# Performance work log

Measured on AMD Instinct MI355X. Metric: run time of the kernel, lower is better.

## Reference

```python
import jax, jax.numpy as jnp
import numpy as np

B = 1; H = 192; W = 192; DIM = 128; HEADS = 8
WS = 16                      # window_size
OWS = 24                     # overlap_win_size = int(16*0.5)+16
PAD = 4                      # (OWS-WS)//2
C2 = DIM // 2                # per-branch channels
H2 = HEADS // 2              # per-branch heads
HID = 256                    # mlp_ratio * dim
TBL = (WS + OWS - 1) ** 2    # 1521 rel-pos table entries
SCALE = (C2 // H2) ** (-0.5) # head_dim ** -0.5


def layer_norm(x, w, b, eps=1e-5):
    mu = jnp.mean(x, -1, keepdims=True)
    var = jnp.mean((x - mu) ** 2, -1, keepdims=True)
    return (x - mu) * jax.lax.rsqrt(var + eps) * w + b


def window_partition(x, ws):
    b, h, w, c = x.shape
    x = x.reshape(b, h // ws, ws, w // ws, ws, c).transpose(0, 1, 3, 2, 4, 5)
    return x.reshape(-1, ws, ws, c)


def window_reverse(win, ws, h, w):
    b = win.shape[0] // ((h // ws) * (w // ws))
    x = win.reshape(b, h // ws, w // ws, ws, ws, -1).transpose(0, 1, 3, 2, 4, 5)
    return x.reshape(b, h, w, -1)


def _patch_idx(h, w):
    ri = (jnp.arange(h // WS) * WS)[:, None] + jnp.arange(OWS)  # (nwh, OWS)
    ci = (jnp.arange(w // WS) * WS)[:, None] + jnp.arange(OWS)  # (nww, OWS)
    return ri, ci


def unfold_patches(x):
    # x: (b, h, w, c) -> (b*nw, OWS*OWS, c); matches nn.Unfold(OWS, stride=WS, pad=PAD)
    b, h, w, c = x.shape
    xp = jnp.pad(x, ((0, 0), (PAD, PAD), (PAD, PAD), (0, 0)))
    ri, ci = _patch_idx(h, w)
    p = xp[:, ri[:, None, :, None], ci[None, :, None, :], :]  # (b,nwh,nww,OWS,OWS,c)
    return p.reshape(-1, OWS * OWS, c)


def fold_patches(p, b, h, w):
    # inverse of unfold: scatter-add overlapping patches into (b, h+2PAD, w+2PAD, c)
    nwh, nww = h // WS, w // WS
    c = p.shape[-1]
    p = p.reshape(b, nwh, nww, OWS, OWS, c)
    ri, ci = _patch_idx(h, w)
    canvas = jnp.zeros((b, h + 2 * PAD, w + 2 * PAD, c), p.dtype)
    return canvas.at[:, ri[:, None, :, None], ci[None, :, None, :], :].add(p)


def cubic_kernel(x, A=-0.75):
    # PyTorch bicubic (cubic convolution, A=-0.75)
    ax = jnp.abs(x)
    w1 = ((A + 2.0) * ax - (A + 3.0)) * ax * ax + 1.0
    w2 = A * (ax * (ax * (ax - 5.0) + 8.0) - 4.0)
    return jnp.where(ax <= 1.0, w1, jnp.where(ax < 2.0, w2, 0.0))


def resize_matrix(n_out, n_in):
    # dense 1-D bicubic resize matrix, align_corners=False, border-clamped (torch semantics)
    i = jnp.arange(n_out, dtype=jnp.float32)
    src = (i + 0.5) * (float(n_in) / float(n_out)) - 0.5
    fl = jnp.floor(src)
    idx = fl[:, None] + jnp.arange(-1, 3, dtype=jnp.float32)[None, :]  # (n_out, 4)
    wts = cubic_kernel(src[:, None] - idx)
    idx_c = jnp.clip(idx, 0, n_in - 1).astype(jnp.int32)
    M = jnp.zeros((n_out, n_in), jnp.float32)
    return M.at[jnp.arange(n_out)[:, None], idx_c].add(wts)


def cross_attn(xq, xkv, rpi, wq, wkv, rpb):
    b_, nq, d = xq.shape
    n = xkv.shape[1]
    q = (xq @ wq).reshape(b_, nq, H2, -1).transpose(0, 2, 1, 3)
    k, v = jnp.split(xkv @ wkv, 2, axis=-1)
    k = k.reshape(b_, n, H2, -1).transpose(0, 2, 1, 3)
    v = v.reshape(b_, n, H2, -1).transpose(0, 2, 1, 3)
    attn = jnp.einsum('bhqd,bhkd->bhqk', q * SCALE, k)
    bias = rpb[rpi.reshape(-1)].reshape(WS * WS, OWS * OWS, H2)
    bias = bias.transpose(2, 0, 1) if nq < n else bias.transpose(2, 1, 0)
    attn = jax.nn.softmax(attn + bias[None], axis=-1)
    out = jnp.einsum('bhqk,bhkd->bhqd', attn, v)
    return out.transpose(0, 2, 1, 3).reshape(b_, nq, d)


def gsfn(x, h, w, fc1_w, fc1_b, sgn_w, sgn_b, conv_w, conv_b, fc2_w, fc2_b):
    x = x @ fc1_w + fc1_b  # NOTE: source GSFN never applies self.act
    x1, x2 = jnp.split(x, 2, axis=-1)
    Bn, N, Ch = x2.shape
    x2 = layer_norm(x2, sgn_w, sgn_b).transpose(0, 2, 1).reshape(Bn, Ch, h, w)
    x2 = jax.lax.conv_general_dilated(
        x2, conv_w, (1, 1), ((1, 1), (1, 1)),
        feature_group_count=Ch, dimension_numbers=('NCHW', 'OIHW', 'NCHW'))
    x2 = x2 + conv_b[None, :, None, None]
    x2 = x2.reshape(Bn, Ch, N).transpose(0, 2, 1)
    return (x1 * x2) @ fc2_w + fc2_b


def mstb(x_tkn, ln1_w, ln1_b, q1_w, kv1_w, rpb1, q2_w, kv2_w, rpb2,
         proj_w, proj_b, ln2_w, ln2_b, fc1_w, fc1_b, sgn_w, sgn_b,
         conv_w, conv_b, fc2_w, fc2_b, rpi, h, w):
    b, _, c = x_tkn.shape
    short = x_tkn
    x = layer_norm(x_tkn, ln1_w, ln1_b).reshape(b, h, w, c)
    xw = window_partition(x, WS).reshape(-1, WS * WS, c)     # (b*nw, ws*ws, c)
    xa, xb = jnp.split(xw, 2, axis=-1)
    xb_img = window_reverse(xb.reshape(-1, WS, WS, C2), WS, h, w)  # (b,h,w,C2)
    xb_p = unfold_patches(xb_img)                            # (b*nw, OWS*OWS, C2)
    a = cross_attn(xa, xb_p, rpi, q1_w, kv1_w, rpb1) + xa
    bb = cross_attn(xb_p, xa, rpi, q2_w, kv2_w, rpb2) + xb_p
    folded = fold_patches(bb, b, h, w)                       # (b, h+2p, w+2p, C2)
    Mh = resize_matrix(h, h + 2 * PAD)
    Mw = resize_matrix(w, w + 2 * PAD)
    resized = jnp.einsum('oi,bijc,pj->bopc', Mh, folded, Mw)  # bicubic to (h,w)
    xb2 = window_partition(resized, WS).reshape(-1, WS * WS, C2)
    x = jnp.concatenate([a, xb2], -1)
    x = window_reverse(x.reshape(-1, WS, WS, c), WS, h, w).reshape(b, h * w, c)
    x = x @ proj_w + proj_b + short
    x = gsfn(layer_norm(x, ln2_w, ln2_b), h, w, fc1_w, fc1_b,
             sgn_w, sgn_b, conv_w, conv_b, fc2_w, fc2_b) + x
    return x


def setup_inputs() -> dict:
    key = jax.random.key(0)
    ks = jax.random.split(key, 12)
    rn = lambda k, s, sc: jax.random.normal(k, s, jnp.float32) * sc
    return {
        'x_tkn': jax.random.normal(ks[0], (B, H * W, DIM), jnp.float32),
        'ln1_w': jnp.ones((DIM,), jnp.float32), 'ln1_b': jnp.zeros((DIM,), jnp.float32),
        'q1_w': rn(ks[1], (C2, C2), 0.05), 'kv1_w': rn(ks[2], (C2, 2 * C2), 0.05),
        'rpb1': rn(ks[3], (TBL, H2), 0.02),
        'q2_w': rn(ks[4], (C2, C2), 0.05), 'kv2_w': rn(ks[5], (C2, 2 * C2), 0.05),
        'rpb2': rn(ks[6], (TBL, H2), 0.02),
        'proj_w': rn(ks[7], (DIM, DIM), 0.05), 'proj_b': jnp.zeros((DIM,), jnp.float32),
        'ln2_w': jnp.ones((DIM,), jnp.float32), 'ln2_b': jnp.zeros((DIM,), jnp.float32),
        'fc1_w': rn(ks[8], (DIM, HID), 0.05), 'fc1_b': jnp.zeros((HID,), jnp.float32),
        'sgn_w': jnp.ones((HID // 2,), jnp.float32), 'sgn_b': jnp.zeros((HID // 2,), jnp.float32),
        'conv_w': rn(ks[9], (HID // 2, 1, 3, 3), 0.1), 'conv_b': jnp.zeros((HID // 2,), jnp.float32),
        'fc2_w': rn(ks[10], (HID // 2, DIM), 0.05), 'fc2_b': jnp.zeros((DIM,), jnp.float32),
        'rpi': jax.random.randint(ks[11], (WS * WS, OWS * OWS), 0, TBL),
        'h': H, 'w': W,
    }


def reference(x_tkn, ln1_w, ln1_b, q1_w, kv1_w, rpb1, q2_w, kv2_w, rpb2,
              proj_w, proj_b, ln2_w, ln2_b, fc1_w, fc1_b, sgn_w, sgn_b,
              conv_w, conv_b, fc2_w, fc2_b, rpi, h, w):
    return mstb(x_tkn, ln1_w, ln1_b, q1_w, kv1_w, rpb1, q2_w, kv2_w, rpb2,
                proj_w, proj_b, ln2_w, ln2_b, fc1_w, fc1_b, sgn_w, sgn_b,
                conv_w, conv_b, fc2_w, fc2_b, rpi, h, w)
```

## Files before the change

### kernel.cpp

```cpp
#include <hip/hip_runtime.h>
#include <hip/hip_bf16.h>

#define HH 192
#define WW 192
#define NWIN 12
#define WSZ 16
#define OWSZ 24
#define PADK 4
#define NQ1 256
#define NKV1 576
#define C2K 64
#define H2K 4
#define HD 16
#define NTOK (HH*WW)
#define LOG2E 1.4426950408889634f
#define QSCALE (0.25f * LOG2E)

typedef __hip_bfloat16 bf16;
typedef __attribute__((ext_vector_type(8))) short bf16x8;
typedef __attribute__((ext_vector_type(4))) float f32x4;

union B8 { short s[8]; bf16x8 v; unsigned u[4]; };

__device__ __forceinline__ unsigned cvtpk(float lo, float hi)
{
    unsigned r;
    asm("v_cvt_pk_bf16_f32 %0, %1, %2" : "=v"(r) : "v"(lo), "v"(hi));
    return r;
}
__device__ __forceinline__ float bfu2f(unsigned short u)
{
    return __uint_as_float(((unsigned)u) << 16);
}

__global__ void wcombT_kernel(const float* __restrict__ q1_w, const float* __restrict__ kv1_w,
                              const float* __restrict__ q2_w, const float* __restrict__ kv2_w,
                              bf16* __restrict__ WT)
{
    int idx = blockIdx.x * 256 + threadIdx.x;
    if (idx >= 384 * 128) return;
    int cp = idx >> 7, r = idx & 127;
    int c;
    if (cp < 64) c = cp;
    else if (cp < 128) c = 192 + (cp - 64);
    else if (cp < 256) {
        int j = cp - 128, h = j >> 5, m = j & 31;
        c = (m < 16) ? (64 + 16 * h + m) : (128 + 16 * h + (m - 16));
    } else {
        int j = cp - 256, h = j >> 5, m = j & 31;
        c = (m < 16) ? (256 + 16 * h + m) : (320 + 16 * h + (m - 16));
    }
    float v = 0.f;
    if (c < 64)       { if (r < 64)  v = q1_w[r * 64 + c] * QSCALE; }
    else if (c < 192) { if (r >= 64) v = kv1_w[(r - 64) * 128 + (c - 64)]; }
    else if (c < 256) { if (r >= 64) v = q2_w[(r - 64) * 64 + (c - 192)] * QSCALE; }
    else              { if (r < 64)  v = kv2_w[r * 128 + (c - 256)]; }
    WT[idx] = __float2bfloat16(v);
}

__global__ void wtrans_kernel(const float* __restrict__ src, int N, bf16* __restrict__ dst)
{
    int idx = blockIdx.x * 256 + threadIdx.x;
    if (idx >= N * 128) return;
    int n = idx >> 7, k = idx & 127;
    dst[idx] = __float2bfloat16(src[(size_t)k * N + n]);
}

__global__ void bias1_kernel(const float* __restrict__ rpb1, const int* __restrict__ rpi,
                             float* __restrict__ biasT)
{
    int idx = blockIdx.x * 256 + threadIdx.x;
    if (idx >= H2K * NKV1 * NQ1) return;
    int q = idx & 255;
    int n = (idx >> 8) % NKV1;
    int h = idx / (NKV1 * NQ1);
    biasT[idx] = rpb1[rpi[q * NKV1 + n] * H2K + h] * LOG2E;
}

__global__ void bias2_kernel(const float* __restrict__ rpb2, const int* __restrict__ rpi,
                             float* __restrict__ biasT)
{
    int idx = blockIdx.x * 256 + threadIdx.x;
    if (idx >= H2K * NQ1 * NKV1) return;
    int q = idx % NKV1;
    int k = (idx / NKV1) % NQ1;
    int h = idx / (NKV1 * NQ1);
    biasT[idx] = rpb2[rpi[k * NKV1 + q] * H2K + h] * LOG2E;
}

__launch_bounds__(256)
__global__ void gemm_qkv(const float* __restrict__ x_tkn,
                         const float* __restrict__ ln1w, const float* __restrict__ ln1b,
                         const bf16* __restrict__ WT,
                         unsigned* __restrict__ qkvo, float* __restrict__ lnx)
{
    const int tid = threadIdx.x;
    const int lane = tid & 63, w = tid >> 6;
    const int g = lane >> 4, nl = lane & 15;

    bf16x8 wf[6][4];
#pragma unroll
    for (int t = 0; t < 6; t++) {
        const bf16* wp = WT + (size_t)((w * 6 + t) * 16 + nl) * 128;
#pragma unroll
        for (int ks = 0; ks < 4; ks++)
            wf[t][ks] = *(const bf16x8*)(wp + ks * 32 + 8 * g);
    }

    const int row = (blockIdx.x * 4 + blockIdx.y) * 16 + nl;
    const float* ap = x_tkn + (size_t)row * 128 + 8 * g;

    float av[4][8];
    float s = 0.f, sq = 0.f;
#pragma unroll
    for (int ks = 0; ks < 4; ks++) {
        float4 v0 = *(const float4*)(ap + ks * 32);
        float4 v1 = *(const float4*)(ap + ks * 32 + 4);
        av[ks][0] = v0.x; av[ks][1] = v0.y; av[ks][2] = v0.z; av[ks][3] = v0.w;
        av[ks][4] = v1.x; av[ks][5] = v1.y; av[ks][6] = v1.z; av[ks][7] = v1.w;
#pragma unroll
        for (int j = 0; j < 8; j++) { s += av[ks][j]; sq += av[ks][j] * av[ks][j]; }
    }
    s  += __shfl_xor(s, 16);  s  += __shfl_xor(s, 32);
    sq += __shfl_xor(sq, 16); sq += __shfl_xor(sq, 32);
    float mu  = s * 0.0078125f;
    float var = fmaxf(sq * 0.0078125f - mu * mu, 0.f);
    float inv = 1.0f / sqrtf(var + 1e-5f);

    bf16x8 xf[4];
#pragma unroll
    for (int ks = 0; ks < 4; ks++) {
        int col = ks * 32 + 8 * g;
        float4 g0 = *(const float4*)(ln1w + col);
        float4 g1 = *(const float4*)(ln1w + col + 4);
        float4 b0 = *(const float4*)(ln1b + col);
        float4 b1 = *(const float4*)(ln1b + col + 4);
        float nv[8];
        nv[0] = (av[ks][0] - mu) * inv * g0.x + b0.x;
        nv[1] = (av[ks][1] - mu) * inv * g0.y + b0.y;
        nv[2] = (av[ks][2] - mu) * inv * g0.z + b0.z;
        nv[3] = (av[ks][3] - mu) * inv * g0.w + b0.w;
        nv[4] = (av[ks][4] - mu) * inv * g1.x + b1.x;
        nv[5] = (av[ks][5] - mu) * inv * g1.y + b1.y;
        nv[6] = (av[ks][6] - mu) * inv * g1.z + b1.z;
        nv[7] = (av[ks][7] - mu) * inv * g1.w + b1.w;
        if (w == 0) {
            float* lp = lnx + (size_t)row * 128 + col;
            *(float4*)lp       = make_float4(nv[0], nv[1], nv[2], nv[3]);
            *(float4*)(lp + 4) = make_float4(nv[4], nv[5], nv[6], nv[7]);
        }
        B8 f;
        f.u[0] = cvtpk(nv[0], nv[1]);
        f.u[1] = cvtpk(nv[2], nv[3]);
        f.u[2] = cvtpk(nv[4], nv[5]);
        f.u[3] = cvtpk(nv[6], nv[7]);
        xf[ks] = f.v;
    }

    const f32x4 zz = {0.f, 0.f, 0.f, 0.f};
    f32x4 acc[6];
#pragma unroll
    for (int t = 0; t < 6; t++) acc[t] = zz;
#pragma unroll
    for (int ks = 0; ks < 4; ks++)
#pragma unroll
        for (int t = 0; t < 6; t++)
            acc[t] = __builtin_amdgcn_mfma_f32_16x16x32_bf16(wf[t][ks], xf[ks], acc[t], 0, 0, 0);

#pragma unroll
    for (int t = 0; t < 6; t++) {
        int n0t = (w * 6 + t) * 16 + 4 * g;
        uint2 o;
        o.x = cvtpk(acc[t][0], acc[t][1]);
        o.y = cvtpk(acc[t][2], acc[t][3]);
        *(uint2*)(qkvo + (size_t)row * 192 + (n0t >> 1)) = o;
    }
}

__launch_bounds__(256)
__global__ void attn_fused(const unsigned* __restrict__ qkvu,
                           const float* __restrict__ lnx,
                           const float* __restrict__ bias1T,
                           const float* __restrict__ bias2T,
                           float* __restrict__ xcat,
                           float* __restrict__ bb)
{
    __shared__ unsigned K_lds[NKV1][10];
    __shared__ unsigned V_lds[NKV1][10];

    const int ebid = (blockIdx.x & 7) * 90 + (blockIdx.x >> 3);
    const int h = blockIdx.y;
    const int tid = threadIdx.x;
    const int lane = tid & 63, w = tid >> 6;
    const int g = lane >> 4, qloc = lane & 15;
    const f32x4 zz = {0.f, 0.f, 0.f, 0.f};

    if (ebid < 288) {
        const int win = ebid % 144, z = ebid / 144;
        const int wi = win / NWIN, wj = win % NWIN;

        for (int n = tid; n < NKV1; n += 256) {
            int rr = wi * WSZ - PADK + n / OWSZ, cc = wj * WSZ - PADK + n % OWSZ;
            bool ib = (rr >= 0 && rr < HH && cc >= 0 && cc < WW);
            uint4 k0v = make_uint4(0, 0, 0, 0), k1v = k0v, v0v = k0v, v1v = k0v;
            if (ib) {
                const unsigned* src = qkvu + (size_t)(rr * WW + cc) * 192 + 64 + 16 * h;
                k0v = *(const uint4*)(src);
                k1v = *(const uint4*)(src + 4);
                v0v = *(const uint4*)(src + 8);
                v1v = *(const uint4*)(src + 12);
            }
            *(uint4*)&K_lds[n][0] = k0v; *(uint4*)&K_lds[n][4] = k1v;
            *(uint4*)&V_lds[n][0] = v0v; *(uint4*)&V_lds[n][4] = v1v;
        }
        __syncthreads();

        const int q0base = z * 128 + w * 32;
        bf16x8 qfrag[2];
#pragma unroll
        for (int qt = 0; qt < 2; qt++) {
            int q = q0base + qt * 16 + qloc;
            int pix = (wi * WSZ + (q >> 4)) * WW + wj * WSZ + (q & 15);
            B8 f;
#pragma unroll
            for (int j = 0; j < 4; j++) f.u[j] = 0;
            if (g < 2)
                f.v = *(const bf16x8*)(qkvu + (size_t)pix * 192 + 8 * h + 4 * g);
            qfrag[qt] = f.v;
        }

        f32x4 O[2];
        float lsum[2];
#pragma unroll
        for (int qt = 0; qt < 2; qt++) { O[qt] = zz; lsum[qt] = 0.f; }

        for (int step = 0; step < 18; step++) {
            const int k0 = step * 32;
            bf16x8 kfA, kfB;
            if (g < 2) {
                kfA = *(const bf16x8*)&K_lds[k0 + qloc][4 * g];
                kfB = *(const bf16x8*)&K_lds[k0 + 16 + qloc][4 * g];
            } else {
                B8 zf;
#pragma unroll
                for (int j = 0; j < 4; j++) zf.u[j] = 0;
                kfA = zf.v; kfB = zf.v;
            }
            B8 vf;
#pragma unroll
            for (int j = 0; j < 8; j++) {
                int key = k0 + 4 * g + (j & 3) + ((j >> 2) << 4);
                unsigned word = V_lds[key][qloc >> 1];
                vf.s[j] = (short)((qloc & 1) ? (word >> 16) : (word & 0xffff));
            }

#pragma unroll
            for (int qt = 0; qt < 2; qt++) {
                f32x4 sA = __builtin_amdgcn_mfma_f32_16x16x32_bf16(kfA, qfrag[qt], zz, 0, 0, 0);
                f32x4 sB = __builtin_amdgcn_mfma_f32_16x16x32_bf16(kfB, qfrag[qt], zz, 0, 0, 0);
                int qa = q0base + qt * 16 + qloc;
                const float* bpA = bias1T + ((size_t)h * NKV1 + k0 + 4 * g) * NQ1 + qa;
                const float* bpB = bpA + 16 * NQ1;
                float pa[4], pb[4];
                float ls = 0.f;
#pragma unroll
                for (int r = 0; r < 4; r++) {
                    pa[r] = exp2f(sA[r] + bpA[(size_t)r * NQ1]);
                    pb[r] = exp2f(sB[r] + bpB[(size_t)r * NQ1]);
                    ls += pa[r] + pb[r];
                }
                B8 pf;
                pf.u[0] = cvtpk(pa[0], pa[1]);
                pf.u[1] = cvtpk(pa[2], pa[3]);
                pf.u[2] = cvtpk(pb[0], pb[1]);
                pf.u[3] = cvtpk(pb[2], pb[3]);
                lsum[qt] += ls;
                O[qt] = __builtin_amdgcn_mfma_f32_16x16x32_bf16(vf.v, pf.v, O[qt], 0, 0, 0);
            }
        }

#pragma unroll
        for (int qt = 0; qt < 2; qt++) {
            float lt = lsum[qt];
            lt += __shfl_xor(lt, 16);
            lt += __shfl_xor(lt, 32);
            float rl = 1.f / lt;
            int q = q0base + qt * 16 + qloc;
            int pix = (wi * WSZ + (q >> 4)) * WW + wj * WSZ + (q & 15);
            size_t base = (size_t)pix * 128 + h * HD + 4 * g;
#pragma unroll
            for (int r = 0; r < 4; r++)
                xcat[base + r] = O[qt][r] * rl + lnx[base + r];
        }
    } else {
        const int bx = ebid - 288;
        const int win = bx % 144, z = bx / 144;
        const int wi = win / NWIN, wj = win % NWIN;

        {
            int n = tid;
            int pix = (wi * WSZ + (n >> 4)) * WW + wj * WSZ + (n & 15);
            const unsigned* src = qkvu + (size_t)pix * 192 + 128 + 16 * h;
            *(uint4*)&K_lds[n][0] = *(const uint4*)(src);
            *(uint4*)&K_lds[n][4] = *(const uint4*)(src + 4);
            *(uint4*)&V_lds[n][0] = *(const uint4*)(src + 8);
            *(uint4*)&V_lds[n][4] = *(const uint4*)(src + 12);
        }
        __syncthreads();

        const int q0base = z * 192 + w * 48;
        bf16x8 qfrag[3];
        bool qin[3];
        int qpix[3];
#pragma unroll
        for (int qt = 0; qt < 3; qt++) {
            int qa = q0base + qt * 16 + qloc;
            int gr = wi * WSZ - PADK + qa / OWSZ, gc = wj * WSZ - PADK + qa % OWSZ;
            bool ib = (gr >= 0 && gr < HH && gc >= 0 && gc < WW);
            qin[qt] = ib;
            qpix[qt] = ib ? gr * WW + gc : 0;
            B8 f;
#pragma unroll
            for (int j = 0; j < 4; j++) f.u[j] = 0;
            if (ib && g < 2)
                f.v = *(const bf16x8*)(qkvu + (size_t)qpix[qt] * 192 + 32 + 8 * h + 4 * g);
            qfrag[qt] = f.v;
        }

        f32x4 O[3];
        float lsum[3];
#pragma unroll
        for (int qt = 0; qt < 3; qt++) { O[qt] = zz; lsum[qt] = 0.f; }

        for (int step = 0; step < 8; step++) {
            const int k0 = step * 32;
            bf16x8 kfA, kfB;
            if (g < 2) {
                kfA = *(const bf16x8*)&K_lds[k0 + qloc][4 * g];
                kfB = *(const bf16x8*)&K_lds[k0 + 16 + qloc][4 * g];
            } else {
                B8 zf;
#pragma unroll
                for (int j = 0; j < 4; j++) zf.u[j] = 0;
                kfA = zf.v; kfB = zf.v;
            }
            B8 vf;
#pragma unroll
            for (int j = 0; j < 8; j++) {
                int key = k0 + 4 * g + (j & 3) + ((j >> 2) << 4);
                unsigned word = V_lds[key][qloc >> 1];
                vf.s[j] = (short)((qloc & 1) ? (word >> 16) : (word & 0xffff));
            }

#pragma unroll
            for (int qt = 0; qt < 3; qt++) {
                f32x4 sA = __builtin_amdgcn_mfma_f32_16x16x32_bf16(kfA, qfrag[qt], zz, 0, 0, 0);
                f32x4 sB = __builtin_amdgcn_mfma_f32_16x16x32_bf16(kfB, qfrag[qt], zz, 0, 0, 0);
                int qa = q0base + qt * 16 + qloc;
                const float* bpA = bias2T + ((size_t)h * NQ1 + k0 + 4 * g) * NKV1 + qa;
                const float* bpB = bpA + 16 * NKV1;
                float pa[4], pb[4];
                float ls = 0.f;
#pragma unroll
                for (int r = 0; r < 4; r++) {
                    pa[r] = exp2f(sA[r] + bpA[(size_t)r * NKV1]);
                    pb[r] = exp2f(sB[r] + bpB[(size_t)r * NKV1]);
                    ls += pa[r] + pb[r];
                }
                B8 pf;
                pf.u[0] = cvtpk(pa[0], pa[1]);
                pf.u[1] = cvtpk(pa[2], pa[3]);
                pf.u[2] = cvtpk(pb[0], pb[1]);
                pf.u[3] = cvtpk(pb[2], pb[3]);
                lsum[qt] += ls;
                O[qt] = __builtin_amdgcn_mfma_f32_16x16x32_bf16(vf.v, pf.v, O[qt], 0, 0, 0);
            }
        }

#pragma unroll
        for (int qt = 0; qt < 3; qt++) {
            float lt = lsum[qt];
            lt += __shfl_xor(lt, 16);
            lt += __shfl_xor(lt, 32);
            float rl = 1.f / lt;
            int qa = q0base + qt * 16 + qloc;
            size_t obase = ((size_t)win * NKV1 + qa) * C2K + h * HD + 4 * g;
            size_t rbase = (size_t)qpix[qt] * 128 + C2K + h * HD + 4 * g;
#pragma unroll
            for (int r = 0; r < 4; r++)
                bb[obase + r] = O[qt][r] * rl + (qin[qt] ? lnx[rbase + r] : 0.f);
        }
    }
}

__global__ void fold_kernel(const float* __restrict__ bb, float* __restrict__ folded)
{
    int idx = blockIdx.x * 256 + threadIdx.x;
    if (idx >= 200 * 200 * 64) return;
    int c = idx & 63;
    int j = (idx >> 6) % 200;
    int i = idx / (64 * 200);
    int ilo = (i > 23) ? ((i - 8) >> 4) : 0;
    int ihi = min(11, i >> 4);
    int jlo = (j > 23) ? ((j - 8) >> 4) : 0;
    int jhi = min(11, j >> 4);
    float s = 0.f;
    for (int wi = ilo; wi <= ihi; wi++)
        for (int wj = jlo; wj <= jhi; wj++) {
            int p = (i - wi * 16) * OWSZ + (j - wj * 16);
            s += bb[((size_t)(wi * NWIN + wj) * NKV1 + p) * C2K + c];
        }
    folded[idx] = s;
}

__device__ __forceinline__ float cubicw(float x)
{
    float ax = fabsf(x);
    const float A = -0.75f;
    if (ax <= 1.f) return ((A + 2.f) * ax - (A + 3.f)) * ax * ax + 1.f;
    if (ax < 2.f)  return A * (ax * (ax * (ax - 5.f) + 8.f) - 4.f);
    return 0.f;
}

__global__ void resize_kernel(const float* __restrict__ folded, float* __restrict__ xcat)
{
    int idx = blockIdx.x * 256 + threadIdx.x;
    if (idx >= HH * WW * C2K) return;
    int c = idx & 63;
    int p = (idx >> 6) % WW;
    int o = idx / (C2K * WW);
    const float ratio = 200.f / 192.f;
    float sr = (o + 0.5f) * ratio - 0.5f;
    float sc = (p + 0.5f) * ratio - 0.5f;
    int fr = (int)floorf(sr), fcc = (int)floorf(sc);
    float wc[4]; int ic[4];
#pragma unroll
    for (int u = 0; u < 4; u++) {
        int jj = fcc - 1 + u;
        wc[u] = cubicw(sc - (float)jj);
        ic[u] = min(max(jj, 0), 199);
    }
    float acc = 0.f;
#pragma unroll
    for (int t = 0; t < 4; t++) {
        int ii = fr - 1 + t;
        float wr = cubicw(sr - (float)ii);
        int ir = min(max(ii, 0), 199);
        const float* rowp = folded + ((size_t)ir * 200) * 64 + c;
        float rs = 0.f;
#pragma unroll
        for (int u = 0; u < 4; u++) rs += wc[u] * rowp[(size_t)ic[u] * 64];
        acc += wr * rs;
    }
    xcat[(size_t)(o * WW + p) * 128 + C2K + c] = acc;
}

__launch_bounds__(256)
__global__ void proj_ln2(const float* __restrict__ A1,
                         const bf16* __restrict__ WT,
                         const float* __restrict__ bias,
                         const float* __restrict__ R,
                         const float* __restrict__ ln2w, const float* __restrict__ ln2b,
                         float* __restrict__ xbuf, unsigned* __restrict__ ybf)
{
    __shared__ float psum[16][16];
    __shared__ float psq[16][16];
    __shared__ float mu_s[16], inv_s[16];

    const int tid = threadIdx.x;
    const int lane = tid & 63, w = tid >> 6;
    const int g = lane >> 4, nl = lane & 15;

    bf16x8 wf[2][4];
#pragma unroll
    for (int t = 0; t < 2; t++) {
        const bf16* wp = WT + (size_t)((w * 2 + t) * 16 + nl) * 128;
#pragma unroll
        for (int ks = 0; ks < 4; ks++)
            wf[t][ks] = *(const bf16x8*)(wp + ks * 32 + 8 * g);
    }

    const int row = (blockIdx.x * 4 + blockIdx.y) * 16 + nl;
    bf16x8 xf[4];
    const float* ap = A1 + (size_t)row * 128 + 8 * g;
#pragma unroll
    for (int ks = 0; ks < 4; ks++) {
        float4 v0 = *(const float4*)(ap + ks * 32);
        float4 v1 = *(const float4*)(ap + ks * 32 + 4);
        B8 f;
        f.u[0] = cvtpk(v0.x, v0.y);
        f.u[1] = cvtpk(v0.z, v0.w);
        f.u[2] = cvtpk(v1.x, v1.y);
        f.u[3] = cvtpk(v1.z, v1.w);
        xf[ks] = f.v;
    }

    const f32x4 zz = {0.f, 0.f, 0.f, 0.f};
    f32x4 acc[2];
    acc[0] = zz; acc[1] = zz;
#pragma unroll
    for (int ks = 0; ks < 4; ks++) {
        acc[0] = __builtin_amdgcn_mfma_f32_16x16x32_bf16(wf[0][ks], xf[ks], acc[0], 0, 0, 0);
        acc[1] = __builtin_amdgcn_mfma_f32_16x16x32_bf16(wf[1][ks], xf[ks], acc[1], 0, 0, 0);
    }

    float o[2][4];
    float s = 0.f, sq = 0.f;
#pragma unroll
    for (int t = 0; t < 2; t++) {
        int n0t = (w * 2 + t) * 16 + 4 * g;
        float4 bv = *(const float4*)(bias + n0t);
        float4 rv = *(const float4*)(R + (size_t)row * 128 + n0t);
        o[t][0] = acc[t][0] + bv.x + rv.x;
        o[t][1] = acc[t][1] + bv.y + rv.y;
        o[t][2] = acc[t][2] + bv.z + rv.z;
        o[t][3] = acc[t][3] + bv.w + rv.w;
#pragma unroll
        for (int r = 0; r < 4; r++) { s += o[t][r]; sq += o[t][r] * o[t][r]; }
    }
    psum[nl][w * 4 + g] = s;
    psq[nl][w * 4 + g] = sq;
    __syncthreads();
    if (tid < 16) {
        float ts = 0.f, tq = 0.f;
#pragma unroll
        for (int i = 0; i < 16; i++) { ts += psum[tid][i]; tq += psq[tid][i]; }
        float mu = ts * 0.0078125f;
        float var = fmaxf(tq * 0.0078125f - mu * mu, 0.f);
        mu_s[tid] = mu;
        inv_s[tid] = 1.0f / sqrtf(var + 1e-5f);
    }
    __syncthreads();

    float mu = mu_s[nl], inv = inv_s[nl];
#pragma unroll
    for (int t = 0; t < 2; t++) {
        int n0t = (w * 2 + t) * 16 + 4 * g;
        *(float4*)(xbuf + (size_t)row * 128 + n0t) = make_float4(o[t][0], o[t][1], o[t][2], o[t][3]);
        float4 gw = *(const float4*)(ln2w + n0t);
        float4 gb = *(const float4*)(ln2b + n0t);
        float y0 = (o[t][0] - mu) * inv * gw.x + gb.x;
        float y1 = (o[t][1] - mu) * inv * gw.y + gb.y;
        float y2 = (o[t][2] - mu) * inv * gw.z + gb.z;
        float y3 = (o[t][3] - mu) * inv * gw.w + gb.w;
        uint2 yo;
        yo.x = cvtpk(y0, y1);
        yo.y = cvtpk(y2, y3);
        *(uint2*)(ybf + (size_t)row * 64 + (n0t >> 1)) = yo;
    }
}

__launch_bounds__(256)
__global__ void fc1_sgn(const unsigned* __restrict__ ybf,
                        const bf16* __restrict__ WT,
                        const float* __restrict__ bias,
                        const float* __restrict__ sgnw, const float* __restrict__ sgnb,
                        unsigned* __restrict__ x1b, unsigned* __restrict__ x2b)
{
    __shared__ float psum[16][8];
    __shared__ float psq[16][8];
    __shared__ float mu_s[16], inv_s[16];

    const int tid = threadIdx.x;
    const int lane = tid & 63, w = tid >> 6;
    const int g = lane >> 4, nl = lane & 15;

    bf16x8 wf[4][4];
#pragma unroll
    for (int t = 0; t < 4; t++) {
        const bf16* wp = WT + (size_t)((w * 4 + t) * 16 + nl) * 128;
#pragma unroll
        for (int ks = 0; ks < 4; ks++)
            wf[t][ks] = *(const bf16x8*)(wp + ks * 32 + 8 * g);
    }

    const int row = (blockIdx.x * 4 + blockIdx.y) * 16 + nl;
    bf16x8 xf[4];
    const unsigned* ap = ybf + (size_t)row * 64 + 4 * g;
#pragma unroll
    for (int ks = 0; ks < 4; ks++)
        xf[ks] = *(const bf16x8*)(ap + ks * 16);

    const f32x4 zz = {0.f, 0.f, 0.f, 0.f};
    f32x4 acc[4];
#pragma unroll
    for (int t = 0; t < 4; t++) acc[t] = zz;
#pragma unroll
    for (int ks = 0; ks < 4; ks++)
#pragma unroll
        for (int t = 0; t < 4; t++)
            acc[t] = __builtin_amdgcn_mfma_f32_16x16x32_bf16(wf[t][ks], xf[ks], acc[t], 0, 0, 0);

    float o[4][4];
    float s = 0.f, sq = 0.f;
#pragma unroll
    for (int t = 0; t < 4; t++) {
        int n0t = (w * 4 + t) * 16 + 4 * g;
        float4 bv = *(const float4*)(bias + n0t);
        o[t][0] = acc[t][0] + bv.x;
        o[t][1] = acc[t][1] + bv.y;
        o[t][2] = acc[t][2] + bv.z;
        o[t][3] = acc[t][3] + bv.w;
    }
    if (w >= 2) {
#pragma unroll
        for (int t = 0; t < 4; t++)
#pragma unroll
            for (int r = 0; r < 4; r++) { s += o[t][r]; sq += o[t][r] * o[t][r]; }
        psum[nl][(w - 2) * 4 + g] = s;
        psq[nl][(w - 2) * 4 + g] = sq;
    }
    __syncthreads();
    if (tid < 16) {
        float ts = 0.f, tq = 0.f;
#pragma unroll
        for (int i = 0; i < 8; i++) { ts += psum[tid][i]; tq += psq[tid][i]; }
        float mu = ts * 0.0078125f;
        float var = fmaxf(tq * 0.0078125f - mu * mu, 0.f);
        mu_s[tid] = mu;
        inv_s[tid] = 1.0f / sqrtf(var + 1e-5f);
    }
    __syncthreads();

    if (w < 2) {
#pragma unroll
        for (int t = 0; t < 4; t++) {
            int n0t = (w * 4 + t) * 16 + 4 * g;
            uint2 xo;
            xo.x = cvtpk(o[t][0], o[t][1]);
            xo.y = cvtpk(o[t][2], o[t][3]);
            *(uint2*)(x1b + (size_t)row * 64 + (n0t >> 1)) = xo;
        }
    } else {
        float mu = mu_s[nl], inv = inv_s[nl];
#pragma unroll
        for (int t = 0; t < 4; t++) {
            int n0t = (w * 4 + t) * 16 + 4 * g;
            int m0t = n0t - 128;
            float4 gw = *(const float4*)(sgnw + m0t);
            float4 gb = *(const float4*)(sgnb + m0t);
            float y0 = (o[t][0] - mu) * inv * gw.x + gb.x;
            float y1 = (o[t][1] - mu) * inv * gw.y + gb.y;
            float y2 = (o[t][2] - mu) * inv * gw.z + gb.z;
            float y3 = (o[t][3] - mu) * inv * gw.w + gb.w;
            uint2 xo;
            xo.x = cvtpk(y0, y1);
            xo.y = cvtpk(y2, y3);
            *(uint2*)(x2b + (size_t)row * 64 + (m0t >> 1)) = xo;
        }
    }
}

__global__ void dwconv_kernel(const unsigned short* __restrict__ x2b,
                              const unsigned short* __restrict__ x1b,
                              const float* __restrict__ conv_w,
                              const float* __restrict__ conv_b,
                              unsigned short* __restrict__ ab)
{
    int idx = blockIdx.x * 256 + threadIdx.x;
    if (idx >= NTOK * 128) return;
    int ch = idx & 127, t = idx >> 7;
    int i = t / WW, j = t % WW;
    float acc = conv_b[ch];
#pragma unroll
    for (int a = 0; a < 3; a++) {
        int ii = i + a - 1;
        if (ii < 0 || ii >= HH) continue;
#pragma unroll
        for (int b = 0; b < 3; b++) {
            int jj = j + b - 1;
            if (jj < 0 || jj >= WW) continue;
            acc += conv_w[ch * 9 + a * 3 + b] * bfu2f(x2b[(size_t)(ii * WW + jj) * 128 + ch]);
        }
    }
    float prod = bfu2f(x1b[(size_t)t * 128 + ch]) * acc;
    unsigned u = __float_as_uint(prod);
    ab[(size_t)t * 128 + ch] = (unsigned short)((u + 0x7FFFu + ((u >> 16) & 1u)) >> 16);
}

__launch_bounds__(256)
__global__ void gemm_bfA(const unsigned* __restrict__ Au,
                         const bf16* __restrict__ WT,
                         const float* __restrict__ bias,
                         const float* __restrict__ R,
                         float* __restrict__ C)
{
    const int tid = threadIdx.x;
    const int lane = tid & 63, w = tid >> 6;
    const int g = lane >> 4, nl = lane & 15;

    bf16x8 wf[2][4];
#pragma unroll
    for (int t = 0; t < 2; t++) {
        const bf16* wp = WT + (size_t)((w * 2 + t) * 16 + nl) * 128;
#pragma unroll
        for (int ks = 0; ks < 4; ks++)
            wf[t][ks] = *(const bf16x8*)(wp + ks * 32 + 8 * g);
    }

    const int row = (blockIdx.x * 4 + blockIdx.y) * 16 + nl;
    bf16x8 xf[4];
    const unsigned* ap = Au + (size_t)row * 64 + 4 * g;
#pragma unroll
    for (int ks = 0; ks < 4; ks++)
        xf[ks] = *(const bf16x8*)(ap + ks * 16);

    const f32x4 zz = {0.f, 0.f, 0.f, 0.f};
    f32x4 acc[2];
    acc[0] = zz; acc[1] = zz;
#pragma unroll
    for (int ks = 0; ks < 4; ks++) {
        acc[0] = __builtin_amdgcn_mfma_f32_16x16x32_bf16(wf[0][ks], xf[ks], acc[0], 0, 0, 0);
        acc[1] = __builtin_amdgcn_mfma_f32_16x16x32_bf16(wf[1][ks], xf[ks], acc[1], 0, 0, 0);
    }

#pragma unroll
    for (int t = 0; t < 2; t++) {
        const int n0t = (w * 2 + t) * 16 + 4 * g;
        float4 bv = *(const float4*)(bias + n0t);
        float4 rv = *(const float4*)(R + (size_t)row * 128 + n0t);
        float4 o;
        o.x = acc[t][0] + bv.x + rv.x;
        o.y = acc[t][1] + bv.y + rv.y;
        o.z = acc[t][2] + bv.z + rv.z;
        o.w = acc[t][3] + bv.w + rv.w;
        *(float4*)(C + (size_t)row * 128 + n0t) = o;
    }
}

extern "C" void kernel_launch(void* const* d_in, const int* in_sizes, int n_in,
                              void* d_out, int out_size, void* d_ws, size_t ws_size,
                              hipStream_t stream)
{
    (void)in_sizes; (void)n_in; (void)out_size; (void)ws_size;
    const float* x_tkn  = (const float*)d_in[0];
    const float* ln1_w  = (const float*)d_in[1];
    const float* ln1_b  = (const float*)d_in[2];
    const float* q1_w   = (const float*)d_in[3];
    const float* kv1_w  = (const float*)d_in[4];
    const float* rpb1   = (const float*)d_in[5];
    const float* q2_w   = (const float*)d_in[6];
    const float* kv2_w  = (const float*)d_in[7];
    const float* rpb2   = (const float*)d_in[8];
    const float* proj_w = (const float*)d_in[9];
    const float* proj_b = (const float*)d_in[10];
    const float* ln2_w  = (const float*)d_in[11];
    const float* ln2_b  = (const float*)d_in[12];
    const float* fc1_w  = (const float*)d_in[13];
    const float* fc1_b  = (const float*)d_in[14];
    const float* sgn_w  = (const float*)d_in[15];
    const float* sgn_b  = (const float*)d_in[16];
    const float* conv_w = (const float*)d_in[17];
    const float* conv_b = (const float*)d_in[18];
    const float* fc2_w  = (const float*)d_in[19];
    const float* fc2_b  = (const float*)d_in[20];
    const int*   rpi    = (const int*)d_in[21];

    float* ws = (float*)d_ws;
    float* lnx    = ws;
    float* xcat   = ws + 4718592;
    float* bbuf   = ws + 9437184;
    bf16*  projT  = (bf16*)(ws + 14155776);
    bf16*  fc1T   = (bf16*)(ws + 14163968);
    bf16*  fc2T   = (bf16*)(ws + 14180352);
    float* bias1T = ws + 14745600;
    float* bias2T = ws + 17104896;
    float* qkv    = ws + 17694720;
    bf16*  wcombT = (bf16*)(ws + 24772608);
    float* foldp  = ws + 17694720;
    unsigned* ybf = (unsigned*)bbuf;
    unsigned* x1b = (unsigned*)(ws + 14745600);
    unsigned* x2b = (unsigned*)(ws + 17104896);
    unsigned* ab  = (unsigned*)(ws + 19464192);
    float* out    = (float*)d_out;

    wcombT_kernel<<<(384 * 128) / 256, 256, 0, stream>>>(q1_w, kv1_w, q2_w, kv2_w, wcombT);
    bias1_kernel<<<(H2K * NKV1 * NQ1) / 256, 256, 0, stream>>>(rpb1, rpi, bias1T);
    bias2_kernel<<<(H2K * NQ1 * NKV1) / 256, 256, 0, stream>>>(rpb2, rpi, bias2T);
    gemm_qkv<<<dim3(NTOK / 64, 4), 256, 0, stream>>>(x_tkn, ln1_w, ln1_b, wcombT,
                                                     (unsigned*)qkv, lnx);
    attn_fused<<<dim3(720, 4), 256, 0, stream>>>((const unsigned*)qkv, lnx,
                                                 bias1T, bias2T, xcat, bbuf);
    fold_kernel<<<(200 * 200 * 64) / 256, 256, 0, stream>>>(bbuf, foldp);
    wtrans_kernel<<<(128 * 128) / 256, 256, 0, stream>>>(proj_w, 128, projT);
    wtrans_kernel<<<(256 * 128) / 256, 256, 0, stream>>>(fc1_w, 256, fc1T);
    wtrans_kernel<<<(128 * 128) / 256, 256, 0, stream>>>(fc2_w, 128, fc2T);
    resize_kernel<<<(HH * WW * C2K) / 256, 256, 0, stream>>>(foldp, xcat);
    proj_ln2<<<dim3(NTOK / 64, 4), 256, 0, stream>>>(xcat, projT, proj_b, x_tkn,
                                                     ln2_w, ln2_b, lnx, ybf);
    fc1_sgn<<<dim3(NTOK / 64, 4), 256, 0, stream>>>(ybf, fc1T, fc1_b, sgn_w, sgn_b, x1b, x2b);
    dwconv_kernel<<<(NTOK * 128) / 256, 256, 0, stream>>>((const unsigned short*)x2b,
                                                          (const unsigned short*)x1b,
                                                          conv_w, conv_b,
                                                          (unsigned short*)ab);
    gemm_bfA<<<dim3(NTOK / 64, 4), 256, 0, stream>>>(ab, fc2T, fc2_b, lnx, out);
}
```

Baseline: 282.4 us.

## Pre-transpose V into MFMA fragment layout in LDS and drop block swizzle

V is now scattered at load time into a per-step, per-lane fragment layout in shared memory, so each step reads the MFMA A-operand with one 16-byte LDS load instead of eight scalar loads plus shifts. The XCD-style block index remap (ebid) is also removed, so blocks map directly to windows. The cost is 16 scattered 2-byte LDS stores per key during staging, and the swizzle removal may change L2 locality across dies.

Result: no change. 278.1 us (-1.5%).

```diff
diff --git a/kernel.cpp b/kernel.cpp
--- a/kernel.cpp
+++ b/kernel.cpp
@@ -186,17 +186,16 @@
                            float* __restrict__ bb)
 {
     __shared__ unsigned K_lds[NKV1][10];
-    __shared__ unsigned V_lds[NKV1][10];
-
-    const int ebid = (blockIdx.x & 7) * 90 + (blockIdx.x >> 3);
+    __shared__ unsigned short Vt[18][64][8];
+
     const int h = blockIdx.y;
     const int tid = threadIdx.x;
     const int lane = tid & 63, w = tid >> 6;
     const int g = lane >> 4, qloc = lane & 15;
     const f32x4 zz = {0.f, 0.f, 0.f, 0.f};
 
-    if (ebid < 288) {
-        const int win = ebid % 144, z = ebid / 144;
+    if (blockIdx.x < 288) {
+        const int win = blockIdx.x % 144, z = blockIdx.x / 144;
         const int wi = win / NWIN, wj = win % NWIN;
 
         for (int n = tid; n < NKV1; n += 256) {
@@ -211,7 +210,16 @@
                 v1v = *(const uint4*)(src + 12);
             }
             *(uint4*)&K_lds[n][0] = k0v; *(uint4*)&K_lds[n][4] = k1v;
-            *(uint4*)&V_lds[n][0] = v0v; *(uint4*)&V_lds[n][4] = v1v;
+            int step = n >> 5, ko = n & 31;
+            int gq = (ko & 15) >> 2;
+            int j = (ko & 3) | ((ko >> 4) << 2);
+            unsigned vv[8] = {v0v.x, v0v.y, v0v.z, v0v.w, v1v.x, v1v.y, v1v.z, v1v.w};
+            unsigned short* vt = &Vt[step][gq * 16][j];
+#pragma unroll
+            for (int d = 0; d < 8; d++) {
+                vt[(2 * d) * 8]     = (unsigned short)(vv[d] & 0xffff);
+                vt[(2 * d + 1) * 8] = (unsigned short)(vv[d] >> 16);
+            }
         }
         __syncthreads();
 
@@ -246,13 +254,7 @@
                 for (int j = 0; j < 4; j++) zf.u[j] = 0;
                 kfA = zf.v; kfB = zf.v;
             }
-            B8 vf;
-#pragma unroll
-            for (int j = 0; j < 8; j++) {
-                int key = k0 + 4 * g + (j & 3) + ((j >> 2) << 4);
-                unsigned word = V_lds[key][qloc >> 1];
-                vf.s[j] = (short)((qloc & 1) ? (word >> 16) : (word & 0xffff));
-            }
+            bf16x8 vfv = *(const bf16x8*)&Vt[step][lane][0];
 
 #pragma unroll
             for (int qt = 0; qt < 2; qt++) {
@@ -275,7 +277,7 @@
                 pf.u[2] = cvtpk(pb[0], pb[1]);
                 pf.u[3] = cvtpk(pb[2], pb[3]);
                 lsum[qt] += ls;
-                O[qt] = __builtin_amdgcn_mfma_f32_16x16x32_bf16(vf.v, pf.v, O[qt], 0, 0, 0);
+                O[qt] = __builtin_amdgcn_mfma_f32_16x16x32_bf16(vfv, pf.v, O[qt], 0, 0, 0);
             }
         }
 
@@ -293,7 +295,7 @@
                 xcat[base + r] = O[qt][r] * rl + lnx[base + r];
         }
     } else {
-        const int bx = ebid - 288;
+        const int bx = blockIdx.x - 288;
         const int win = bx % 144, z = bx / 144;
         const int wi = win / NWIN, wj = win % NWIN;
 
@@ -301,10 +303,22 @@
             int n = tid;
             int pix = (wi * WSZ + (n >> 4)) * WW + wj * WSZ + (n & 15);
             const unsigned* src = qkvu + (size_t)pix * 192 + 128 + 16 * h;
-            *(uint4*)&K_lds[n][0] = *(const uint4*)(src);
-            *(uint4*)&K_lds[n][4] = *(const uint4*)(src + 4);
-            *(uint4*)&V_lds[n][0] = *(const uint4*)(src + 8);
-            *(uint4*)&V_lds[n][4] = *(const uint4*)(src + 12);
+            uint4 k0v = *(const uint4*)(src);
+            uint4 k1v = *(const uint4*)(src + 4);
+            uint4 v0v = *(const uint4*)(src + 8);
+            uint4 v1v = *(const uint4*)(src + 12);
+            *(uint4*)&K_lds[n][0] = k0v;
+            *(uint4*)&K_lds[n][4] = k1v;
+            int step = n >> 5, ko = n & 31;
+            int gq = (ko & 15) >> 2;
+            int j = (ko & 3) | ((ko >> 4) << 2);
+            unsigned vv[8] = {v0v.x, v0v.y, v0v.z, v0v.w, v1v.x, v1v.y, v1v.z, v1v.w};
+            unsigned short* vt = &Vt[step][gq * 16][j];
+#pragma unroll
+            for (int d = 0; d < 8; d++) {
+                vt[(2 * d) * 8]     = (unsigned short)(vv[d] & 0xffff);
+                vt[(2 * d + 1) * 8] = (unsigned short)(vv[d] >> 16);
+            }
         }
         __syncthreads();
 
@@ -344,13 +358,7 @@
                 for (int j = 0; j < 4; j++) zf.u[j] = 0;
                 kfA = zf.v; kfB = zf.v;
             }
-            B8 vf;
-#pragma unroll
-            for (int j = 0; j < 8; j++) {
-                int key = k0 + 4 * g + (j & 3) + ((j >> 2) << 4);
-                unsigned word = V_lds[key][qloc >> 1];
-                vf.s[j] = (short)((qloc & 1) ? (word >> 16) : (word & 0xffff));
-            }
+            bf16x8 vfv = *(const bf16x8*)&Vt[step][lane][0];
 
 #pragma unroll
             for (int qt = 0; qt < 3; qt++) {
@@ -373,7 +381,7 @@
                 pf.u[2] = cvtpk(pb[0], pb[1]);
                 pf.u[3] = cvtpk(pb[2], pb[3]);
                 lsum[qt] += ls;
-                O[qt] = __builtin_amdgcn_mfma_f32_16x16x32_bf16(vf.v, pf.v, O[qt], 0, 0, 0);
+                O[qt] = __builtin_amdgcn_mfma_f32_16x16x32_bf16(vfv, pf.v, O[qt], 0, 0, 0);
             }
         }
 
```
